# Kernel tuning notes

Measured on AMD Instinct MI355X. Metric: run time of the kernel, lower is better.

Reference implementation:

```python
import jax, jax.numpy as jnp
import numpy as np

D, H, HD, F, A, P, NB, MD = 1024, 16, 64, 2816, 64, 30, 32, 128
B, L = 4, 1024


def _rel_bucket(rel, num_buckets=NB, max_distance=MD):
    # T5 relative position bucket, bidirectional=False (decoder self-attn)
    rel = -jnp.minimum(rel, 0)
    max_exact = num_buckets // 2
    is_small = rel < max_exact
    large = max_exact + (
        jnp.log(jnp.maximum(rel, 1).astype(jnp.float32) / max_exact)
        / np.log(max_distance / max_exact)
        * (num_buckets - max_exact)
    ).astype(jnp.int32)
    large = jnp.minimum(large, num_buckets - 1)
    return jnp.where(is_small, rel, large)


def _rmsnorm(x, scale, eps=1e-6):
    var = jnp.mean(jnp.square(x), axis=-1, keepdims=True)
    return x * jax.lax.rsqrt(var + eps) * scale


def _attn(x, kv, wq, wk, wv, wo, mask, bias, pk, pv):
    # x: [B,Lq,D], kv: [B,Lk,D], prefix pk/pv: [B,P,H,HD]
    hd = wq.shape[-1]
    q = jnp.einsum('bqd,dhe->bqhe', x, wq) * (hd ** -0.5)
    k = jnp.einsum('bkd,dhe->bkhe', kv, wk)
    v = jnp.einsum('bkd,dhe->bkhe', kv, wv)
    k = jnp.concatenate([pk, k], axis=1)  # prefix KV prepended
    v = jnp.concatenate([pv, v], axis=1)
    logits = jnp.einsum('bqhe,bkhe->bhqk', q, k).astype(jnp.float32)
    p = pk.shape[1]
    if bias is not None:
        logits = logits + jnp.pad(bias, ((0, 0), (0, 0), (0, 0), (p, 0)))
    mask = jnp.pad(mask, ((0, 0), (0, 0), (0, 0), (p, 0)), constant_values=True)
    logits = jnp.where(mask, logits, jnp.float32(-1e10))
    w = jax.nn.softmax(logits, axis=-1).astype(x.dtype)
    o = jnp.einsum('bhqk,bkhe->bqhe', w, v)
    return jnp.einsum('bqhe,hed->bqd', o, wo)


def setup_inputs() -> dict:
    key = jax.random.key(0)
    ks = jax.random.split(key, 24)
    s = D ** -0.5
    inp = {
        'inputs': jax.random.normal(ks[0], (B, L, D), jnp.float32),
        'encoded': jax.random.normal(ks[1], (B, L, D), jnp.float32),
        'adapter_wd': jax.random.normal(ks[2], (B, D, A), jnp.float32) * s,
        'adapter_wu': jax.random.normal(ks[3], (B, A, D), jnp.float32) * (A ** -0.5),
        'adapter_bd': jax.random.normal(ks[4], (B, A), jnp.float32) * 0.02,
        'adapter_bu': jax.random.normal(ks[5], (B, D), jnp.float32) * 0.02,
        'prefix_key': jax.random.normal(ks[6], (B, 2, P, H, HD), jnp.float32),
        'prefix_value': jax.random.normal(ks[7], (B, 2, P, H, HD), jnp.float32),
        'ln1': jnp.ones((D,), jnp.float32),
        'ln2': jnp.ones((D,), jnp.float32),
        'ln3': jnp.ones((D,), jnp.float32),
        'sa_wq': jax.random.normal(ks[8], (D, H, HD), jnp.float32) * s,
        'sa_wk': jax.random.normal(ks[9], (D, H, HD), jnp.float32) * s,
        'sa_wv': jax.random.normal(ks[10], (D, H, HD), jnp.float32) * s,
        'sa_wo': jax.random.normal(ks[11], (H, HD, D), jnp.float32) * s,
        'ca_wq': jax.random.normal(ks[12], (D, H, HD), jnp.float32) * s,
        'ca_wk': jax.random.normal(ks[13], (D, H, HD), jnp.float32) * s,
        'ca_wv': jax.random.normal(ks[14], (D, H, HD), jnp.float32) * s,
        'ca_wo': jax.random.normal(ks[15], (H, HD, D), jnp.float32) * s,
        'relpos': jax.random.normal(ks[16], (H, NB), jnp.float32) * 0.1,
        'mlp_wi0': jax.random.normal(ks[17], (D, F), jnp.float32) * s,
        'mlp_wi1': jax.random.normal(ks[18], (D, F), jnp.float32) * s,
        'mlp_wo': jax.random.normal(ks[19], (F, D), jnp.float32) * (F ** -0.5),
        'decoder_mask': jnp.broadcast_to(jnp.tril(jnp.ones((L, L), bool))[None, None], (B, 1, L, L)),
        'encoder_decoder_mask': jnp.ones((B, 1, L, L), bool),
    }
    return inp


def reference(inputs, encoded, adapter_wd, adapter_wu, adapter_bd, adapter_bu,
              prefix_key, prefix_value, ln1, ln2, ln3,
              sa_wq, sa_wk, sa_wv, sa_wo, ca_wq, ca_wk, ca_wv, ca_wo,
              relpos, mlp_wi0, mlp_wi1, mlp_wo,
              decoder_mask, encoder_decoder_mask):
    l = inputs.shape[1]
    pos = jnp.arange(l)
    buckets = _rel_bucket(pos[None, :] - pos[:, None])  # [L,L]
    bias = relpos[:, buckets][None]                      # [1,H,L,L]
    # self-attention with prefix + relative bias
    x = _rmsnorm(inputs, ln1)
    x = _attn(x, x, sa_wq, sa_wk, sa_wv, sa_wo, decoder_mask, bias,
              prefix_key[:, 0], prefix_value[:, 0])
    x = x + inputs
    # cross-attention with prefix
    y = _rmsnorm(x, ln2)
    y = _attn(y, encoded, ca_wq, ca_wk, ca_wv, ca_wo, encoder_decoder_mask, None,
              prefix_key[:, 1], prefix_value[:, 1])
    y = y + x
    # gated-gelu MLP + per-example adapter
    lz = _rmsnorm(y, ln3)
    z = (jax.nn.gelu(lz @ mlp_wi0) * (lz @ mlp_wi1)) @ mlp_wo
    az = jnp.einsum('bld,bda->bla', lz, adapter_wd) + adapter_bd[:, None]
    az = jax.nn.gelu(az)
    az = jnp.einsum('bla,bad->bld', az, adapter_wu) + adapter_bu[:, None]
    z = z + az
    return z + y
```

## Files before the change

### kernel.cpp

```cpp
#include <hip/hip_runtime.h>

typedef unsigned short u16;
typedef __attribute__((ext_vector_type(8))) __bf16 bf16x8;
typedef __attribute__((ext_vector_type(4))) float f32x4;

__device__ __forceinline__ float bf2f(u16 u) {
  union { unsigned int i; float f; } v; v.i = ((unsigned int)u) << 16; return v.f;
}
__device__ __forceinline__ u16 f2bf(float f) {
  unsigned int x = __float_as_uint(f);
  unsigned int r = (x + 0x7fffu + ((x >> 16) & 1u)) >> 16;
  return (u16)r;
}
__device__ __forceinline__ u16 f2bf_fast(float f) {
  return (u16)((__float_as_uint(f) + 0x8000u) >> 16);
}
__device__ __forceinline__ float gelu_f(float x) {
  float u = 0.7978845608028654f * (x + 0.044715f * x * x * x);
  float t = 1.0f - 2.0f / (__expf(2.0f * u) + 1.0f);
  return 0.5f * x * (1.0f + t);
}
__device__ __forceinline__ void gl_lds16(const u16* g, u16* l) {
  __builtin_amdgcn_global_load_lds(
      (const __attribute__((address_space(1))) unsigned int*)g,
// ... 18 lines not shown
  out += (size_t)blockIdx.z * osb;
  int c0 = blockIdx.x * 32, r0 = blockIdx.y * 32;
  int tx = threadIdx.x & 31, ty = threadIdx.x >> 5;
#pragma unroll
  for (int i = 0; i < 4; ++i) {
    int rr = r0 + ty + i * 8;
    if (rr < R && c0 + tx < C) tile[ty + i * 8][tx] = f2bf(in[(size_t)rr * C + c0 + tx]);
  }
  __syncthreads();
#pragma unroll
  for (int i = 0; i < 4; ++i) {
    int cc = c0 + ty + i * 8;
    if (cc < C && r0 + tx < R) out[(size_t)cc * R + r0 + tx] = tile[tx][ty + i * 8];
  }
}

__global__ __launch_bounds__(256) void bias_tab_k(const float* __restrict__ relpos,
                                                  float* __restrict__ tab) {
  int idx = blockIdx.x * 256 + threadIdx.x;
  int h = idx >> 10, d = idx & 1023;
  int bucket;
  if (d < 16) bucket = d;
  else {
    int lb = 16 + (int)(logf((float)d * (1.0f / 16.0f)) * (16.0f / logf(8.0f)));
    bucket = lb < 31 ? lb : 31;
  }
  tab[idx] = relpos[h * 32 + bucket];
}

__global__ __launch_bounds__(256) void prefix_fill_k(
    const float* __restrict__ pK, const float* __restrict__ pV,
    u16* __restrict__ Kd, u16* __restrict__ Vtd, int sSel) {
  int idx = blockIdx.x * 256 + threadIdx.x;
  int e = idx & 63, p = (idx >> 6) & 31, h = (idx >> 11) & 15, b = idx >> 15;
  int key = (p < 30) ? p : (1024 + p);
  float kv = 0.f, vv = 0.f;
  if (p < 30) {
    size_t src = ((((size_t)(b * 2 + sSel)) * 30 + p) * 16 + h) * 64 + e;
    kv = pK[src]; vv = pV[src];
  }
  Kd[(((size_t)(b * 16 + h)) * 1056 + key) * 64 + e] = f2bf(kv);
  Vtd[(((size_t)(b * 16 + h)) * 64 + e) * 1056 + key] = f2bf(vv);
}

__global__ __launch_bounds__(256) void rmsnorm_k(const float* __restrict__ in,
                                                 const float* __restrict__ scale,
                                                 u16* __restrict__ out) {
  const int D = 1024;
  size_t base = (size_t)blockIdx.x * D;
  int t = threadIdx.x;
  float x[4];
#pragma unroll
  for (int i = 0; i < 4; ++i) x[i] = in[base + t + i * 256];
  float s = x[0] * x[0] + x[1] * x[1] + x[2] * x[2] + x[3] * x[3];
#pragma unroll
  for (int off = 1; off < 64; off <<= 1) s += __shfl_xor(s, off, 64);
  __shared__ float ws4[4];
  if ((t & 63) == 0) ws4[t >> 6] = s;
  __syncthreads();
  float tot = ws4[0] + ws4[1] + ws4[2] + ws4[3];
  float r = rsqrtf(tot * (1.0f / D) + 1e-6f);
#pragma unroll
  for (int i = 0; i < 4; ++i) {
    int c = t + i * 256;
    out[base + c] = f2bf(x[i] * r * scale[c]);
  }
}

__global__ __launch_bounds__(256) void gelumul_k(const u16* __restrict__ g2,
                                                 u16* __restrict__ g) {
  int i = blockIdx.x * 256 + threadIdx.x;
  int m = i / 352, f8 = i - m * 352;
  size_t b0 = (size_t)m * 5632 + f8 * 8;
  uint4 h0 = *(const uint4*)(g2 + b0);
  uint4 h1 = *(const uint4*)(g2 + b0 + 2816);
// ... 51 lines not shown
      bf[j] = *(const bf16x8*)&Bs[(wn + j * 16 + fr) * 32 + fq * 8];
#pragma unroll
    for (int i = 0; i < 4; ++i)
#pragma unroll
      for (int j = 0; j < 4; ++j)
        acc[i * 4 + j] = __builtin_amdgcn_mfma_f32_16x16x32_bf16(
            af[i], bf[j], acc[i * 4 + j], 0, 0, 0);
    __syncthreads();
  }

#pragma unroll
  for (int i = 0; i < 4; ++i) {
#pragma unroll
    for (int rr = 0; rr < 4; ++rr) {
      long gm = (long)m0 + wm + i * 16 + fq * 4 + rr;
#pragma unroll
      for (int j = 0; j < 4; ++j) {
        int gn = n0 + wn + j * 16 + fr;
        float v = acc[i * 4 + j][rr];
        size_t oi = (size_t)gm * N + gn;
        if (MODE == 0) ((float*)out)[oi] = v;
        if (MODE == 2) ((u16*)out)[oi] = f2bf(v);
        if (MODE == 3) ((float*)out)[oi] = v + res1[oi];
        if (MODE == 8) {
          int b = (int)(gm >> 10), l = (int)(gm & 1023), h = gn >> 6, e = gn & 63;
          ((u16*)out)[(((size_t)(b * 16 + h)) * 1024 + l) * 64 + e] = f2bf(v * alpha);
        }
        if (MODE == 11) {
          int b = (int)(gm >> 10), l = (int)(gm & 1023);
          int sec = gn >> 10, nn = gn & 1023, h = nn >> 6, e = nn & 63;
          if (sec == 0)
            ((u16*)out)[(((size_t)(b * 16 + h)) * 1024 + l) * 64 + e] = f2bf(v * alpha);
          else if (sec == 1)
            ((u16*)out2)[(((size_t)(b * 16 + h)) * 1056 + 30 + l) * 64 + e] = f2bf(v);
          else
            ((u16*)out3)[(((size_t)(b * 16 + h)) * 64 + e) * 1056 + 30 + l] = f2bf(v);
        }
        if (MODE == 12) {
          int b = (int)(gm >> 10), l = (int)(gm & 1023);
          int sec = gn >> 10, nn = gn & 1023, h = nn >> 6, e = nn & 63;
          if (sec == 0)
            ((u16*)out)[(((size_t)(b * 16 + h)) * 1056 + 30 + l) * 64 + e] = f2bf(v);
          else
            ((u16*)out2)[(((size_t)(b * 16 + h)) * 64 + e) * 1056 + 30 + l] = f2bf(v);
        }
      }
    }
  }
}

template <int MODE>
__global__ __launch_bounds__(256) void gemm_bt(
    const u16* __restrict__ A, const u16* __restrict__ Bt, void* __restrict__ out,
    const float* __restrict__ res1, const float* __restrict__ res2,
    const float* __restrict__ bias, int M, int N, int K,
    long Asb, long Bsb, long bsb, long r1sb, long r2sb, long osb) {
  const int BM = 128, BK = 32, LP = 40;
  __shared__ __align__(16) u16 As[BM * LP];
  __shared__ __align__(16) u16 Bs[BM * LP];

  const int t = threadIdx.x;
  const int m0 = blockIdx.y * BM;
  const int n0 = blockIdx.x * 128;
  const int bz = blockIdx.z;
  A += (size_t)bz * Asb;
  Bt += (size_t)bz * Bsb;

  f32x4 acc[16];
#pragma unroll
  for (int i = 0; i < 16; ++i) acc[i] = (f32x4){0.f, 0.f, 0.f, 0.f};
  const int wave = t >> 6, lane = t & 63;
  const int wm = (wave >> 1) * 64, wn = (wave & 1) * 64;
  const int fr = lane & 15, fq = lane >> 4;

  for (int k0 = 0; k0 < K; k0 += BK) {
#pragma unroll
    for (int i = 0; i < 2; ++i) {
// ... 18 lines not shown
#pragma unroll
      for (int j = 0; j < 4; ++j)
        acc[i * 4 + j] = __builtin_amdgcn_mfma_f32_16x16x32_bf16(
            af[i], bfr[j], acc[i * 4 + j], 0, 0, 0);
    __syncthreads();
  }

#pragma unroll
  for (int i = 0; i < 4; ++i) {
#pragma unroll
    for (int rr = 0; rr < 4; ++rr) {
      long gm = (long)m0 + wm + i * 16 + fq * 4 + rr;
#pragma unroll
      for (int j = 0; j < 4; ++j) {
        int gn = n0 + wn + j * 16 + fr;
        if (gn >= N) continue;
        float v = acc[i * 4 + j][rr];
        size_t oi = (size_t)bz * osb + (size_t)gm * N + gn;
        size_t ri = (size_t)gm * N + gn;
        if (MODE == 6) ((u16*)out)[oi] = f2bf(gelu_f(v + bias[(size_t)bz * bsb + gn]));
        if (MODE == 7)
          ((float*)out)[oi] = v + bias[(size_t)bz * bsb + gn] +
                              res1[(size_t)bz * r1sb + ri] +
                              res2[(size_t)bz * r2sb + ri];
      }
    }
  }
}

template <bool IS_SELF>
__global__ __launch_bounds__(256) void fattn_k(
    const u16* __restrict__ Qg, const u16* __restrict__ Kg,
    const u16* __restrict__ Vtg, const float* __restrict__ bias_tab,
    u16* __restrict__ Out) {
  const int L = 1024, P = 30, KC = 1056;
  const int b = blockIdx.z, h = blockIdx.y, q0b = blockIdx.x * 64;
  const int t = threadIdx.x, wave = t >> 6, lane = t & 63;
  const int fr = lane & 15, fq = lane >> 4;
  const int q0w = q0b + wave * 16;

  __shared__ float bTs[IS_SELF ? 1024 : 4];
  __shared__ __align__(16) u16 Ps[4][16][40];

  if (IS_SELF) {
#pragma unroll
    for (int i = 0; i < 4; ++i) bTs[t + i * 256] = bias_tab[h * 1024 + t + i * 256];
    __syncthreads();
  }

  const u16* qptr = Qg + (((size_t)(b * 16 + h)) * L + q0w + fr) * 64 + fq * 8;
  bf16x8 qa0 = *(const bf16x8*)qptr;
  bf16x8 qa1 = *(const bf16x8*)(qptr + 32);

  f32x4 o[4];
#pragma unroll
  for (int i = 0; i < 4; ++i) o[i] = (f32x4){0.f, 0.f, 0.f, 0.f};
  f32x4 ol = (f32x4){0.f, 0.f, 0.f, 0.f};
  bf16x8 ones;
  {
    u16 one = 0x3F80;
#pragma unroll
    for (int i = 0; i < 8; ++i) ((u16*)&ones)[i] = one;
  }

  const int nk = IS_SELF ? (P + q0b + 64) : (P + L);
  const int nch = (nk + 31) >> 5;
  const u16* kp = Kg + ((size_t)(b * 16 + h)) * KC * 64 + (size_t)fr * 64 + fq * 8;
  const u16* vp = Vtg + ((size_t)(b * 16 + h)) * 64 * KC + (size_t)fr * KC + fq * 8;

  bf16x8 kf0 = *(const bf16x8*)(kp + 0);
  bf16x8 kf1 = *(const bf16x8*)(kp + 32);
  bf16x8 kf2 = *(const bf16x8*)(kp + 16 * 64);
  bf16x8 kf3 = *(const bf16x8*)(kp + 16 * 64 + 32);

  for (int ch = 0; ch < nch; ++ch) {
    const int k0 = ch * 32;
    bf16x8 vf0 = *(const bf16x8*)(vp + 0 * 16 * KC + k0);
    bf16x8 vf1 = *(const bf16x8*)(vp + 1 * 16 * KC + k0);
    bf16x8 vf2 = *(const bf16x8*)(vp + 2 * 16 * KC + k0);
    bf16x8 vf3 = *(const bf16x8*)(vp + 3 * 16 * KC + k0);
    const int k0n = (ch + 1 < nch) ? (k0 + 32) : 0;
    bf16x8 kn0 = *(const bf16x8*)(kp + (size_t)k0n * 64);
    bf16x8 kn1 = *(const bf16x8*)(kp + (size_t)k0n * 64 + 32);
    bf16x8 kn2 = *(const bf16x8*)(kp + (size_t)(k0n + 16) * 64);
    bf16x8 kn3 = *(const bf16x8*)(kp + (size_t)(k0n + 16) * 64 + 32);

    f32x4 s[2];
    s[0] = (f32x4){0.f, 0.f, 0.f, 0.f};
    s[1] = (f32x4){0.f, 0.f, 0.f, 0.f};
    s[0] = __builtin_amdgcn_mfma_f32_16x16x32_bf16(qa0, kf0, s[0], 0, 0, 0);
    s[0] = __builtin_amdgcn_mfma_f32_16x16x32_bf16(qa1, kf1, s[0], 0, 0, 0);
    s[1] = __builtin_amdgcn_mfma_f32_16x16x32_bf16(qa0, kf2, s[1], 0, 0, 0);
    s[1] = __builtin_amdgcn_mfma_f32_16x16x32_bf16(qa1, kf3, s[1], 0, 0, 0);

    const bool full = IS_SELF ? (k0 >= 32 && k0 + 31 - P <= q0w)
                              : (k0 + 31 < P + L);
    if (full) {
      if (IS_SELF) {
#pragma unroll
        for (int reg = 0; reg < 4; ++reg) {
          const int qq = q0w + fq * 4 + reg;
          s[0][reg] += bTs[qq - (k0 + fr - P)];
          s[1][reg] += bTs[qq - (k0 + 16 + fr - P)];
        }
      }
    } else {
#pragma unroll
      for (int reg = 0; reg < 4; ++reg) {
        const int qq = q0w + fq * 4 + reg;
#pragma unroll
        for (int t2 = 0; t2 < 2; ++t2) {
          const int kvi = k0 + t2 * 16 + fr;
          float sv = s[t2][reg];
          if (IS_SELF) {
            const int lk = kvi - P;
            if (lk >= 0) {
              if (lk <= qq) sv += bTs[qq - lk];
              else sv = -3.0e38f;
            }
          } else {
            if (kvi >= P + L) sv = -3.0e38f;
          }
          s[t2][reg] = sv;
        }
      }
    }

#pragma unroll
    for (int reg = 0; reg < 4; ++reg) {
      Ps[wave][fq * 4 + reg][fr] = f2bf_fast(__expf(s[0][reg]));
      Ps[wave][fq * 4 + reg][16 + fr] = f2bf_fast(__expf(s[1][reg]));
    }
    __asm__ volatile("s_waitcnt lgkmcnt(0)" ::: "memory");
    bf16x8 pa = *(const bf16x8*)&Ps[wave][fr][fq * 8];

    o[0] = __builtin_amdgcn_mfma_f32_16x16x32_bf16(pa, vf0, o[0], 0, 0, 0);
    o[1] = __builtin_amdgcn_mfma_f32_16x16x32_bf16(pa, vf1, o[1], 0, 0, 0);
    o[2] = __builtin_amdgcn_mfma_f32_16x16x32_bf16(pa, vf2, o[2], 0, 0, 0);
    o[3] = __builtin_amdgcn_mfma_f32_16x16x32_bf16(pa, vf3, o[3], 0, 0, 0);
    ol   = __builtin_amdgcn_mfma_f32_16x16x32_bf16(pa, ones, ol, 0, 0, 0);

    kf0 = kn0; kf1 = kn1; kf2 = kn2; kf3 = kn3;
  }

  float inv[4];
#pragma unroll
  for (int reg = 0; reg < 4; ++reg) inv[reg] = 1.0f / ol[reg];
#pragma unroll
  for (int dt = 0; dt < 4; ++dt) {
#pragma unroll
    for (int reg = 0; reg < 4; ++reg) {
      size_t oidx =
          (((size_t)(b * L + q0w + fq * 4 + reg)) * 16 + h) * 64 + dt * 16 + fr;
      Out[oidx] = f2bf(o[dt][reg] * inv[reg]);
    }
  }
}

extern "C" void kernel_launch(void* const* d_in, const int* in_sizes, int n_in,
                              void* d_out, int out_size, void* d_ws, size_t ws_size,
                              hipStream_t stream) {
  const int B = 4, L = 1024, D = 1024, H = 16, F = 2816, AD = 64;
  const int M = B * L;
  const int KC = 1056;

  const float* inputs  = (const float*)d_in[0];
  const float* encoded = (const float*)d_in[1];
  const float* a_wd    = (const float*)d_in[2];
  const float* a_wu    = (const float*)d_in[3];
  const float* a_bd    = (const float*)d_in[4];
  const float* a_bu    = (const float*)d_in[5];
  const float* pK      = (const float*)d_in[6];
  const float* pV      = (const float*)d_in[7];
  const float* ln1     = (const float*)d_in[8];
  const float* ln2     = (const float*)d_in[9];
  const float* ln3     = (const float*)d_in[10];
  const float* sa_wq   = (const float*)d_in[11];
  const float* sa_wk   = (const float*)d_in[12];
  const float* sa_wv   = (const float*)d_in[13];
  const float* sa_wo   = (const float*)d_in[14];
  const float* ca_wq   = (const float*)d_in[15];
  const float* ca_wk   = (const float*)d_in[16];
  const float* ca_wv   = (const float*)d_in[17];
  const float* ca_wo   = (const float*)d_in[18];
  const float* relpos  = (const float*)d_in[19];
  const float* wi0     = (const float*)d_in[20];
  const float* wi1     = (const float*)d_in[21];
  const float* wom     = (const float*)d_in[22];

  char* w = (char*)d_ws;
  size_t used = 0;
  auto alloc = [&](size_t bytes) {
    char* p = w + used;
    used += (bytes + 255) & ~(size_t)255;
    return p;
  };
  u16* wqkvT  = (u16*)alloc((size_t)3072 * 1024 * 2);
  u16* woT    = (u16*)alloc((size_t)D * 1024 * 2);
  u16* cqT    = (u16*)alloc((size_t)D * 1024 * 2);
  u16* ckvT   = (u16*)alloc((size_t)2048 * 1024 * 2);
  u16* coT    = (u16*)alloc((size_t)D * 1024 * 2);
  u16* wi01T  = (u16*)alloc((size_t)5632 * 1024 * 2);
  u16* womT   = (u16*)alloc((size_t)D * F * 2);
  u16* wdT    = (u16*)alloc((size_t)B * AD * D * 2);
  u16* wuT    = (u16*)alloc((size_t)B * D * AD * 2);
  float* bT   = (float*)alloc((size_t)H * 1024 * 4);
  u16* enc16  = (u16*)alloc((size_t)M * D * 2);
  u16* xn     = (u16*)alloc((size_t)M * D * 2);
  u16* lz     = (u16*)alloc((size_t)M * D * 2);
  u16* Kc     = (u16*)alloc((size_t)B * H * KC * 64 * 2);
  u16* Vtc    = (u16*)alloc((size_t)B * H * 64 * KC * 2);
  u16* qh     = (u16*)alloc((size_t)B * H * L * 64 * 2);
  u16* ao     = (u16*)alloc((size_t)M * D * 2);
  float* xf   = (float*)alloc((size_t)M * D * 4);
  float* yf   = (float*)alloc((size_t)M * D * 4);
  u16* az1    = (u16*)alloc((size_t)B * 1024 * AD * 2);
  u16* g2     = Kc;
  u16* g      = enc16;
  float* zf   = (float*)Kc;
  if (used > ws_size) return;

  dim3 tb(256);
  auto T = [&](const float* src, u16* dst, int R, int C, int nb, long sb) {
    transpose_k<<<dim3((C + 31) / 32, (R + 31) / 32, nb), tb, 0, stream>>>(
        src, dst, R, C, sb, sb);
  };
  T(sa_wq, wqkvT, D, 1024, 1, 0);
  T(sa_wk, wqkvT + (size_t)1024 * 1024, D, 1024, 1, 0);
  T(sa_wv, wqkvT + (size_t)2048 * 1024, D, 1024, 1, 0);
  T(sa_wo, woT, 1024, D, 1, 0);
  T(ca_wq, cqT, D, 1024, 1, 0);
  T(ca_wk, ckvT, D, 1024, 1, 0);
  T(ca_wv, ckvT + (size_t)1024 * 1024, D, 1024, 1, 0);
  T(ca_wo, coT, 1024, D, 1, 0);
  T(wi0, wi01T, D, F, 1, 0);
  T(wi1, wi01T + (size_t)2816 * 1024, D, F, 1, 0);
  T(wom, womT, F, D, 1, 0);
  T(a_wd, wdT, D, AD, B, (long)D * AD);
  T(a_wu, wuT, AD, D, B, (long)AD * D);
  bias_tab_k<<<dim3(64), tb, 0, stream>>>(relpos, bT);
  cast_bf16_k<<<dim3(M * D / 4 / 256), tb, 0, stream>>>(encoded, enc16, M * D / 4);

#define G97(MODE, Ap, Btp, Op, O2, O3, R1, Nn, Kk, al)                         \
  gemm97<MODE><<<dim3((Nn) / 128, M / 128), tb, 0, stream>>>(                  \
      (const u16*)(Ap), (const u16*)(Btp), (void*)(Op), (void*)(O2),           \
      (void*)(O3), (const float*)(R1), M, Nn, Kk, al)

  rmsnorm_k<<<dim3(M), tb, 0, stream>>>(inputs, ln1, xn);
  G97(11, xn, wqkvT, qh, Kc, Vtc, nullptr, 3072, D, 0.125f);
  prefix_fill_k<<<dim3(512), tb, 0, stream>>>(pK, pV, Kc, Vtc, 0);
  fattn_k<true><<<dim3(L / 64, H, B), tb, 0, stream>>>(qh, Kc, Vtc, bT, ao);
  G97(3, ao, woT, xf, nullptr, nullptr, inputs, 1024, D, 1.f);
  rmsnorm_k<<<dim3(M), tb, 0, stream>>>(xf, ln2, xn);
  G97(8, xn, cqT, qh, nullptr, nullptr, nullptr, 1024, D, 0.125f);
  G97(12, enc16, ckvT, Kc, Vtc, nullptr, nullptr, 2048, D, 1.f);
  prefix_fill_k<<<dim3(512), tb, 0, stream>>>(pK, pV, Kc, Vtc, 1);
  fattn_k<false><<<dim3(L / 64, H, B), tb, 0, stream>>>(qh, Kc, Vtc, nullptr, ao);
  G97(3, ao, coT, yf, nullptr, nullptr, xf, 1024, D, 1.f);
  rmsnorm_k<<<dim3(M), tb, 0, stream>>>(yf, ln3, lz);
  gemm_bt<6><<<dim3(1, 8, B), tb, 0, stream>>>(
      lz, wdT, az1, nullptr, nullptr, a_bd, 1024, AD, D,
      (long)1024 * D, (long)AD * D, (long)AD, 0, 0, (long)1024 * AD);
  G97(2, lz, wi01T, g2, nullptr, nullptr, nullptr, 5632, D, 1.f);
  gelumul_k<<<dim3(5632), tb, 0, stream>>>(g2, g);
  G97(0, g, womT, zf, nullptr, nullptr, nullptr, 1024, F, 1.f);
  gemm_bt<7><<<dim3(8, 8, B), tb, 0, stream>>>(
      az1, wuT, d_out, zf, yf, a_bu, 1024, 1024, AD,
      (long)1024 * AD, (long)D * AD, (long)1024, (long)1024 * 1024,
      (long)1024 * 1024, (long)1024 * 1024);
#undef G97
  (void)in_sizes; (void)n_in; (void)out_size;
}
```

Measured before the change: 828.1 us.

## Process 64-key chunks in flash attention with MFMA priority and XCD-aware block swizzle

The attention kernel now handles two 32-key sub-chunks per iteration. That doubles the in-flight K/V register loads and MFMA work per loop trip, and the P staging buffer is double-buffered in LDS. K/V padding grows from 1056 to 1088 keys so the 64-wide chunks stay in bounds, and the prefix fill and GEMM epilogues change to match. It also adds s_setprio around the MFMA groups and remaps a flat 1D grid so that blocks of the same batch/head land on the same XCD for L2 reuse. The costs are higher register pressure and extra padded work on the last chunk.

Result: slower. 873.8 us (+5.5%).

```diff
diff --git a/kernel.cpp b/kernel.cpp
--- a/kernel.cpp
+++ b/kernel.cpp
@@ -74,15 +74,15 @@
     const float* __restrict__ pK, const float* __restrict__ pV,
     u16* __restrict__ Kd, u16* __restrict__ Vtd, int sSel) {
   int idx = blockIdx.x * 256 + threadIdx.x;
-  int e = idx & 63, p = (idx >> 6) & 31, h = (idx >> 11) & 15, b = idx >> 15;
+  int e = idx & 63, p = (idx >> 6) & 63, h = (idx >> 12) & 15, b = idx >> 16;
   int key = (p < 30) ? p : (1024 + p);
   float kv = 0.f, vv = 0.f;
   if (p < 30) {
     size_t src = ((((size_t)(b * 2 + sSel)) * 30 + p) * 16 + h) * 64 + e;
     kv = pK[src]; vv = pV[src];
   }
-  Kd[(((size_t)(b * 16 + h)) * 1056 + key) * 64 + e] = f2bf(kv);
-  Vtd[(((size_t)(b * 16 + h)) * 64 + e) * 1056 + key] = f2bf(vv);
+  Kd[(((size_t)(b * 16 + h)) * 1088 + key) * 64 + e] = f2bf(kv);
+  Vtd[(((size_t)(b * 16 + h)) * 64 + e) * 1088 + key] = f2bf(vv);
 }
 
 __global__ __launch_bounds__(256) void rmsnorm_k(const float* __restrict__ in,
@@ -200,17 +200,17 @@
           if (sec == 0)
             ((u16*)out)[(((size_t)(b * 16 + h)) * 1024 + l) * 64 + e] = f2bf(v * alpha);
           else if (sec == 1)
-            ((u16*)out2)[(((size_t)(b * 16 + h)) * 1056 + 30 + l) * 64 + e] = f2bf(v);
+            ((u16*)out2)[(((size_t)(b * 16 + h)) * 1088 + 30 + l) * 64 + e] = f2bf(v);
           else
-            ((u16*)out3)[(((size_t)(b * 16 + h)) * 64 + e) * 1056 + 30 + l] = f2bf(v);
+            ((u16*)out3)[(((size_t)(b * 16 + h)) * 64 + e) * 1088 + 30 + l] = f2bf(v);
         }
         if (MODE == 12) {
           int b = (int)(gm >> 10), l = (int)(gm & 1023);
           int sec = gn >> 10, nn = gn & 1023, h = nn >> 6, e = nn & 63;
           if (sec == 0)
-            ((u16*)out)[(((size_t)(b * 16 + h)) * 1056 + 30 + l) * 64 + e] = f2bf(v);
+            ((u16*)out)[(((size_t)(b * 16 + h)) * 1088 + 30 + l) * 64 + e] = f2bf(v);
           else
-            ((u16*)out2)[(((size_t)(b * 16 + h)) * 64 + e) * 1056 + 30 + l] = f2bf(v);
+            ((u16*)out2)[(((size_t)(b * 16 + h)) * 64 + e) * 1088 + 30 + l] = f2bf(v);
         }
       }
     }
@@ -296,14 +296,17 @@
     const u16* __restrict__ Qg, const u16* __restrict__ Kg,
     const u16* __restrict__ Vtg, const float* __restrict__ bias_tab,
     u16* __restrict__ Out) {
-  const int L = 1024, P = 30, KC = 1056;
-  const int b = blockIdx.z, h = blockIdx.y, q0b = blockIdx.x * 64;
+  const int L = 1024, P = 30, KC = 1088;
+  const int flat = blockIdx.x;
+  const int wg = (flat & 7) * 128 + (flat >> 3);
+  const int q0b = (wg & 15) * 64;
+  const int h = (wg >> 4) & 15, b = wg >> 8;
   const int t = threadIdx.x, wave = t >> 6, lane = t & 63;
   const int fr = lane & 15, fq = lane >> 4;
   const int q0w = q0b + wave * 16;
 
   __shared__ float bTs[IS_SELF ? 1024 : 4];
-  __shared__ __align__(16) u16 Ps[4][16][40];
+  __shared__ __align__(16) u16 Ps[4][2][16][40];
 
   if (IS_SELF) {
 #pragma unroll
@@ -327,44 +330,29 @@
   }
 
   const int nk = IS_SELF ? (P + q0b + 64) : (P + L);
-  const int nch = (nk + 31) >> 5;
+  const int nit = (nk + 63) >> 6;
   const u16* kp = Kg + ((size_t)(b * 16 + h)) * KC * 64 + (size_t)fr * 64 + fq * 8;
   const u16* vp = Vtg + ((size_t)(b * 16 + h)) * 64 * KC + (size_t)fr * KC + fq * 8;
 
-  bf16x8 kf0 = *(const bf16x8*)(kp + 0);
-  bf16x8 kf1 = *(const bf16x8*)(kp + 32);
-  bf16x8 kf2 = *(const bf16x8*)(kp + 16 * 64);
-  bf16x8 kf3 = *(const bf16x8*)(kp + 16 * 64 + 32);
-
-  for (int ch = 0; ch < nch; ++ch) {
-    const int k0 = ch * 32;
-    bf16x8 vf0 = *(const bf16x8*)(vp + 0 * 16 * KC + k0);
-    bf16x8 vf1 = *(const bf16x8*)(vp + 1 * 16 * KC + k0);
-    bf16x8 vf2 = *(const bf16x8*)(vp + 2 * 16 * KC + k0);
-    bf16x8 vf3 = *(const bf16x8*)(vp + 3 * 16 * KC + k0);
-    const int k0n = (ch + 1 < nch) ? (k0 + 32) : 0;
-    bf16x8 kn0 = *(const bf16x8*)(kp + (size_t)k0n * 64);
-    bf16x8 kn1 = *(const bf16x8*)(kp + (size_t)k0n * 64 + 32);
-    bf16x8 kn2 = *(const bf16x8*)(kp + (size_t)(k0n + 16) * 64);
-    bf16x8 kn3 = *(const bf16x8*)(kp + (size_t)(k0n + 16) * 64 + 32);
-
-    f32x4 s[2];
-    s[0] = (f32x4){0.f, 0.f, 0.f, 0.f};
-    s[1] = (f32x4){0.f, 0.f, 0.f, 0.f};
-    s[0] = __builtin_amdgcn_mfma_f32_16x16x32_bf16(qa0, kf0, s[0], 0, 0, 0);
-    s[0] = __builtin_amdgcn_mfma_f32_16x16x32_bf16(qa1, kf1, s[0], 0, 0, 0);
-    s[1] = __builtin_amdgcn_mfma_f32_16x16x32_bf16(qa0, kf2, s[1], 0, 0, 0);
-    s[1] = __builtin_amdgcn_mfma_f32_16x16x32_bf16(qa1, kf3, s[1], 0, 0, 0);
-
-    const bool full = IS_SELF ? (k0 >= 32 && k0 + 31 - P <= q0w)
-                              : (k0 + 31 < P + L);
+  bf16x8 ka0 = *(const bf16x8*)(kp + 0);
+  bf16x8 ka1 = *(const bf16x8*)(kp + 32);
+  bf16x8 ka2 = *(const bf16x8*)(kp + 16 * 64);
+  bf16x8 ka3 = *(const bf16x8*)(kp + 16 * 64 + 32);
+  bf16x8 kb0 = *(const bf16x8*)(kp + 32 * 64);
+  bf16x8 kb1 = *(const bf16x8*)(kp + 32 * 64 + 32);
+  bf16x8 kb2 = *(const bf16x8*)(kp + 48 * 64);
+  bf16x8 kb3 = *(const bf16x8*)(kp + 48 * 64 + 32);
+
+  auto smax = [&](f32x4* s, int kk0, int cidx) {
+    const bool full = IS_SELF ? (kk0 >= 32 && kk0 + 31 - P <= q0w)
+                              : (kk0 + 31 < P + L);
     if (full) {
       if (IS_SELF) {
 #pragma unroll
         for (int reg = 0; reg < 4; ++reg) {
           const int qq = q0w + fq * 4 + reg;
-          s[0][reg] += bTs[qq - (k0 + fr - P)];
-          s[1][reg] += bTs[qq - (k0 + 16 + fr - P)];
+          s[0][reg] += bTs[qq - (kk0 + fr - P)];
+          s[1][reg] += bTs[qq - (kk0 + 16 + fr - P)];
         }
       }
     } else {
@@ -373,7 +361,7 @@
         const int qq = q0w + fq * 4 + reg;
 #pragma unroll
         for (int t2 = 0; t2 < 2; ++t2) {
-          const int kvi = k0 + t2 * 16 + fr;
+          const int kvi = kk0 + t2 * 16 + fr;
           float sv = s[t2][reg];
           if (IS_SELF) {
             const int lk = kvi - P;
@@ -388,22 +376,68 @@
         }
       }
     }
-
 #pragma unroll
     for (int reg = 0; reg < 4; ++reg) {
-      Ps[wave][fq * 4 + reg][fr] = f2bf_fast(__expf(s[0][reg]));
-      Ps[wave][fq * 4 + reg][16 + fr] = f2bf_fast(__expf(s[1][reg]));
+      Ps[wave][cidx][fq * 4 + reg][fr] = f2bf_fast(__expf(s[0][reg]));
+      Ps[wave][cidx][fq * 4 + reg][16 + fr] = f2bf_fast(__expf(s[1][reg]));
     }
+  };
+
+  for (int it = 0; it < nit; ++it) {
+    const int k0 = it * 64;
+    bf16x8 va0 = *(const bf16x8*)(vp + 0 * 16 * KC + k0);
+    bf16x8 va1 = *(const bf16x8*)(vp + 1 * 16 * KC + k0);
+    bf16x8 va2 = *(const bf16x8*)(vp + 2 * 16 * KC + k0);
+    bf16x8 va3 = *(const bf16x8*)(vp + 3 * 16 * KC + k0);
+    bf16x8 vb0 = *(const bf16x8*)(vp + 0 * 16 * KC + k0 + 32);
+    bf16x8 vb1 = *(const bf16x8*)(vp + 1 * 16 * KC + k0 + 32);
+    bf16x8 vb2 = *(const bf16x8*)(vp + 2 * 16 * KC + k0 + 32);
+    bf16x8 vb3 = *(const bf16x8*)(vp + 3 * 16 * KC + k0 + 32);
+
+    f32x4 sA[2], sB[2];
+    sA[0] = (f32x4){0.f, 0.f, 0.f, 0.f};
+    sA[1] = (f32x4){0.f, 0.f, 0.f, 0.f};
+    sB[0] = (f32x4){0.f, 0.f, 0.f, 0.f};
+    sB[1] = (f32x4){0.f, 0.f, 0.f, 0.f};
+    __builtin_amdgcn_s_setprio(1);
+    sA[0] = __builtin_amdgcn_mfma_f32_16x16x32_bf16(qa0, ka0, sA[0], 0, 0, 0);
+    sA[0] = __builtin_amdgcn_mfma_f32_16x16x32_bf16(qa1, ka1, sA[0], 0, 0, 0);
+    sA[1] = __builtin_amdgcn_mfma_f32_16x16x32_bf16(qa0, ka2, sA[1], 0, 0, 0);
+    sA[1] = __builtin_amdgcn_mfma_f32_16x16x32_bf16(qa1, ka3, sA[1], 0, 0, 0);
+    sB[0] = __builtin_amdgcn_mfma_f32_16x16x32_bf16(qa0, kb0, sB[0], 0, 0, 0);
+    sB[0] = __builtin_amdgcn_mfma_f32_16x16x32_bf16(qa1, kb1, sB[0], 0, 0, 0);
+    sB[1] = __builtin_amdgcn_mfma_f32_16x16x32_bf16(qa0, kb2, sB[1], 0, 0, 0);
+    sB[1] = __builtin_amdgcn_mfma_f32_16x16x32_bf16(qa1, kb3, sB[1], 0, 0, 0);
+    __builtin_amdgcn_s_setprio(0);
+
+    const int k0n = (it + 1 < nit) ? (k0 + 64) : 0;
+    ka0 = *(const bf16x8*)(kp + (size_t)k0n * 64);
+    ka1 = *(const bf16x8*)(kp + (size_t)k0n * 64 + 32);
+    ka2 = *(const bf16x8*)(kp + (size_t)(k0n + 16) * 64);
+    ka3 = *(const bf16x8*)(kp + (size_t)(k0n + 16) * 64 + 32);
+    kb0 = *(const bf16x8*)(kp + (size_t)(k0n + 32) * 64);
+    kb1 = *(const bf16x8*)(kp + (size_t)(k0n + 32) * 64 + 32);
+    kb2 = *(const bf16x8*)(kp + (size_t)(k0n + 48) * 64);
+    kb3 = *(const bf16x8*)(kp + (size_t)(k0n + 48) * 64 + 32);
+
+    smax(sA, k0, 0);
+    smax(sB, k0 + 32, 1);
     __asm__ volatile("s_waitcnt lgkmcnt(0)" ::: "memory");
-    bf16x8 pa = *(const bf16x8*)&Ps[wave][fr][fq * 8];
-
-    o[0] = __builtin_amdgcn_mfma_f32_16x16x32_bf16(pa, vf0, o[0], 0, 0, 0);
-    o[1] = __builtin_amdgcn_mfma_f32_16x16x32_bf16(pa, vf1, o[1], 0, 0, 0);
-    o[2] = __builtin_amdgcn_mfma_f32_16x16x32_bf16(pa, vf2, o[2], 0, 0, 0);
-    o[3] = __builtin_amdgcn_mfma_f32_16x16x32_bf16(pa, vf3, o[3], 0, 0, 0);
-    ol   = __builtin_amdgcn_mfma_f32_16x16x32_bf16(pa, ones, ol, 0, 0, 0);
-
-    kf0 = kn0; kf1 = kn1; kf2 = kn2; kf3 = kn3;
+    bf16x8 paA = *(const bf16x8*)&Ps[wave][0][fr][fq * 8];
+    bf16x8 paB = *(const bf16x8*)&Ps[wave][1][fr][fq * 8];
+
+    __builtin_amdgcn_s_setprio(1);
+    o[0] = __builtin_amdgcn_mfma_f32_16x16x32_bf16(paA, va0, o[0], 0, 0, 0);
+    o[1] = __builtin_amdgcn_mfma_f32_16x16x32_bf16(paA, va1, o[1], 0, 0, 0);
+    o[2] = __builtin_amdgcn_mfma_f32_16x16x32_bf16(paA, va2, o[2], 0, 0, 0);
+    o[3] = __builtin_amdgcn_mfma_f32_16x16x32_bf16(paA, va3, o[3], 0, 0, 0);
+    ol   = __builtin_amdgcn_mfma_f32_16x16x32_bf16(paA, ones, ol, 0, 0, 0);
+    o[0] = __builtin_amdgcn_mfma_f32_16x16x32_bf16(paB, vb0, o[0], 0, 0, 0);
+    o[1] = __builtin_amdgcn_mfma_f32_16x16x32_bf16(paB, vb1, o[1], 0, 0, 0);
+    o[2] = __builtin_amdgcn_mfma_f32_16x16x32_bf16(paB, vb2, o[2], 0, 0, 0);
+    o[3] = __builtin_amdgcn_mfma_f32_16x16x32_bf16(paB, vb3, o[3], 0, 0, 0);
+    ol   = __builtin_amdgcn_mfma_f32_16x16x32_bf16(paB, ones, ol, 0, 0, 0);
+    __builtin_amdgcn_s_setprio(0);
   }
 
   float inv[4];
@@ -425,7 +459,7 @@
                               hipStream_t stream) {
   const int B = 4, L = 1024, D = 1024, H = 16, F = 2816, AD = 64;
   const int M = B * L;
-  const int KC = 1056;
+  const int KC = 1088;
 
   const float* inputs  = (const float*)d_in[0];
   const float* encoded = (const float*)d_in[1];
@@ -511,14 +545,14 @@
 
   rmsnorm_k<<<dim3(M), tb, 0, stream>>>(inputs, ln1, xn);
   G97(11, xn, wqkvT, qh, Kc, Vtc, nullptr, 3072, D, 0.125f);
-  prefix_fill_k<<<dim3(512), tb, 0, stream>>>(pK, pV, Kc, Vtc, 0);
-  fattn_k<true><<<dim3(L / 64, H, B), tb, 0, stream>>>(qh, Kc, Vtc, bT, ao);
+  prefix_fill_k<<<dim3(1024), tb, 0, stream>>>(pK, pV, Kc, Vtc, 0);
+  fattn_k<true><<<dim3(1024), tb, 0, stream>>>(qh, Kc, Vtc, bT, ao);
   G97(3, ao, woT, xf, nullptr, nullptr, inputs, 1024, D, 1.f);
   rmsnorm_k<<<dim3(M), tb, 0, stream>>>(xf, ln2, xn);
   G97(8, xn, cqT, qh, nullptr, nullptr, nullptr, 1024, D, 0.125f);
   G97(12, enc16, ckvT, Kc, Vtc, nullptr, nullptr, 2048, D, 1.f);
-  prefix_fill_k<<<dim3(512), tb, 0, stream>>>(pK, pV, Kc, Vtc, 1);
-  fattn_k<false><<<dim3(L / 64, H, B), tb, 0, stream>>>(qh, Kc, Vtc, nullptr, ao);
+  prefix_fill_k<<<dim3(1024), tb, 0, stream>>>(pK, pV, Kc, Vtc, 1);
+  fattn_k<false><<<dim3(1024), tb, 0, stream>>>(qh, Kc, Vtc, nullptr, ao);
   G97(3, ao, coT, yf, nullptr, nullptr, xf, 1024, D, 1.f);
   rmsnorm_k<<<dim3(M), tb, 0, stream>>>(yf, ln3, lz);
   gemm_bt<6><<<dim3(1, 8, B), tb, 0, stream>>>(
```

## Split attention key range across two workgroups and merge partials in a combine kernel

Applied to the files above, without the earlier changes.

Each attention workgroup now covers only half of the key chunks for its query tile. It writes unnormalized fp32 partial outputs and row sums to scratch, and a new combine kernel adds the two halves, normalizes, and stores bf16. This doubles the grid and evens out the causal work imbalance in self-attention. Block indices are also remapped (an XCD-style swizzle) so neighbouring tiles share caches. The cost is extra fp32 traffic and one more launch per attention. Partial buffers reuse other workspace regions, and the xn buffer is smaller than the partial output it now holds, so that buffer spills into the adjacent allocation.

After: 831.6 us. Within noise of the previous version (+0.4%).

```diff
diff --git a/kernel.cpp b/kernel.cpp
--- a/kernel.cpp
+++ b/kernel.cpp
@@ -295,12 +295,19 @@
 __global__ __launch_bounds__(256) void fattn_k(
     const u16* __restrict__ Qg, const u16* __restrict__ Kg,
     const u16* __restrict__ Vtg, const float* __restrict__ bias_tab,
-    u16* __restrict__ Out) {
+    float* __restrict__ o0P, float* __restrict__ o1P,
+    float* __restrict__ l0P, float* __restrict__ l1P) {
   const int L = 1024, P = 30, KC = 1056;
-  const int b = blockIdx.z, h = blockIdx.y, q0b = blockIdx.x * 64;
+  const int flat = blockIdx.x;
+  const int wg = (flat & 7) * 256 + (flat >> 3);
+  const int half = wg & 1;
+  const int q0b = ((wg >> 1) & 15) * 64;
+  const int h = (wg >> 5) & 15, b = wg >> 9;
   const int t = threadIdx.x, wave = t >> 6, lane = t & 63;
   const int fr = lane & 15, fq = lane >> 4;
   const int q0w = q0b + wave * 16;
+  float* __restrict__ oP = half ? o1P : o0P;
+  float* __restrict__ lP = half ? l1P : l0P;
 
   __shared__ float bTs[IS_SELF ? 1024 : 4];
   __shared__ __align__(16) u16 Ps[4][16][40];
@@ -327,22 +334,25 @@
   }
 
   const int nk = IS_SELF ? (P + q0b + 64) : (P + L);
-  const int nch = (nk + 31) >> 5;
+  const int ncht = (nk + 31) >> 5;
+  const int c0 = half ? (ncht >> 1) : 0;
+  const int c1 = half ? ncht : (ncht >> 1);
   const u16* kp = Kg + ((size_t)(b * 16 + h)) * KC * 64 + (size_t)fr * 64 + fq * 8;
   const u16* vp = Vtg + ((size_t)(b * 16 + h)) * 64 * KC + (size_t)fr * KC + fq * 8;
 
-  bf16x8 kf0 = *(const bf16x8*)(kp + 0);
-  bf16x8 kf1 = *(const bf16x8*)(kp + 32);
-  bf16x8 kf2 = *(const bf16x8*)(kp + 16 * 64);
-  bf16x8 kf3 = *(const bf16x8*)(kp + 16 * 64 + 32);
-
-  for (int ch = 0; ch < nch; ++ch) {
+  const int kb = c0 * 32;
+  bf16x8 kf0 = *(const bf16x8*)(kp + (size_t)kb * 64);
+  bf16x8 kf1 = *(const bf16x8*)(kp + (size_t)kb * 64 + 32);
+  bf16x8 kf2 = *(const bf16x8*)(kp + (size_t)(kb + 16) * 64);
+  bf16x8 kf3 = *(const bf16x8*)(kp + (size_t)(kb + 16) * 64 + 32);
+
+  for (int ch = c0; ch < c1; ++ch) {
     const int k0 = ch * 32;
     bf16x8 vf0 = *(const bf16x8*)(vp + 0 * 16 * KC + k0);
     bf16x8 vf1 = *(const bf16x8*)(vp + 1 * 16 * KC + k0);
     bf16x8 vf2 = *(const bf16x8*)(vp + 2 * 16 * KC + k0);
     bf16x8 vf3 = *(const bf16x8*)(vp + 3 * 16 * KC + k0);
-    const int k0n = (ch + 1 < nch) ? (k0 + 32) : 0;
+    const int k0n = (ch + 1 < c1) ? (k0 + 32) : 0;
     bf16x8 kn0 = *(const bf16x8*)(kp + (size_t)k0n * 64);
     bf16x8 kn1 = *(const bf16x8*)(kp + (size_t)k0n * 64 + 32);
     bf16x8 kn2 = *(const bf16x8*)(kp + (size_t)(k0n + 16) * 64);
@@ -406,18 +416,42 @@
     kf0 = kn0; kf1 = kn1; kf2 = kn2; kf3 = kn3;
   }
 
-  float inv[4];
-#pragma unroll
-  for (int reg = 0; reg < 4; ++reg) inv[reg] = 1.0f / ol[reg];
 #pragma unroll
   for (int dt = 0; dt < 4; ++dt) {
 #pragma unroll
     for (int reg = 0; reg < 4; ++reg) {
       size_t oidx =
-          (((size_t)(b * L + q0w + fq * 4 + reg)) * 16 + h) * 64 + dt * 16 + fr;
-      Out[oidx] = f2bf(o[dt][reg] * inv[reg]);
+          (((size_t)(b * 16 + h)) * 1024 + q0w + fq * 4 + reg) * 64 + dt * 16 + fr;
+      oP[oidx] = o[dt][reg];
     }
   }
+  if (fr == 0) {
+#pragma unroll
+    for (int reg = 0; reg < 4; ++reg)
+      lP[((size_t)(b * 16 + h)) * 1024 + q0w + fq * 4 + reg] = ol[reg];
+  }
+}
+
+__global__ __launch_bounds__(256) void attn_comb_k(
+    const float* __restrict__ o0, const float* __restrict__ o1,
+    const float* __restrict__ l0, const float* __restrict__ l1,
+    u16* __restrict__ Out) {
+  const int bh = blockIdx.x >> 6;
+  const int q0 = (blockIdx.x & 63) * 16;
+  const int t = threadIdx.x;
+  const int qi = q0 + (t >> 4), dq = (t & 15) * 4;
+  const size_t row = (size_t)bh * 1024 + qi;
+  const size_t src = row * 64 + dq;
+  float4 a = *(const float4*)(o0 + src);
+  float4 c = *(const float4*)(o1 + src);
+  float inv = 1.0f / (l0[row] + l1[row]);
+  ushort4 ov;
+  ov.x = f2bf((a.x + c.x) * inv);
+  ov.y = f2bf((a.y + c.y) * inv);
+  ov.z = f2bf((a.z + c.z) * inv);
+  ov.w = f2bf((a.w + c.w) * inv);
+  const int bb = bh >> 4, hh = bh & 15;
+  *(ushort4*)(Out + ((((size_t)bb * 1024 + qi) * 16 + hh) * 64 + dq)) = ov;
 }
 
 extern "C" void kernel_launch(void* const* d_in, const int* in_sizes, int n_in,
@@ -481,6 +515,10 @@
   u16* g2     = Kc;
   u16* g      = enc16;
   float* zf   = (float*)Kc;
+  float* oh0  = yf;
+  float* oh1  = (float*)xn;
+  float* lh0  = (float*)az1;
+  float* lh1  = lh0 + 65536;
   if (used > ws_size) return;
 
   dim3 tb(256);
@@ -512,13 +550,15 @@
   rmsnorm_k<<<dim3(M), tb, 0, stream>>>(inputs, ln1, xn);
   G97(11, xn, wqkvT, qh, Kc, Vtc, nullptr, 3072, D, 0.125f);
   prefix_fill_k<<<dim3(512), tb, 0, stream>>>(pK, pV, Kc, Vtc, 0);
-  fattn_k<true><<<dim3(L / 64, H, B), tb, 0, stream>>>(qh, Kc, Vtc, bT, ao);
+  fattn_k<true><<<dim3(2048), tb, 0, stream>>>(qh, Kc, Vtc, bT, oh0, oh1, lh0, lh1);
+  attn_comb_k<<<dim3(4096), tb, 0, stream>>>(oh0, oh1, lh0, lh1, ao);
   G97(3, ao, woT, xf, nullptr, nullptr, inputs, 1024, D, 1.f);
   rmsnorm_k<<<dim3(M), tb, 0, stream>>>(xf, ln2, xn);
   G97(8, xn, cqT, qh, nullptr, nullptr, nullptr, 1024, D, 0.125f);
   G97(12, enc16, ckvT, Kc, Vtc, nullptr, nullptr, 2048, D, 1.f);
   prefix_fill_k<<<dim3(512), tb, 0, stream>>>(pK, pV, Kc, Vtc, 1);
-  fattn_k<false><<<dim3(L / 64, H, B), tb, 0, stream>>>(qh, Kc, Vtc, nullptr, ao);
+  fattn_k<false><<<dim3(2048), tb, 0, stream>>>(qh, Kc, Vtc, nullptr, oh0, oh1, lh0, lh1);
+  attn_comb_k<<<dim3(4096), tb, 0, stream>>>(oh0, oh1, lh0, lh1, ao);
   G97(3, ao, coT, yf, nullptr, nullptr, xf, 1024, D, 1.f);
   rmsnorm_k<<<dim3(M), tb, 0, stream>>>(yf, ln3, lz);
   gemm_bt<6><<<dim3(1, 8, B), tb, 0, stream>>>(
```

## Process 32 query rows per wave in flash attention and remap block order

Applied to the files above, without the earlier changes.

Each wave now handles two 16-row query tiles that share every K and V fragment load, so K/V global traffic per query is halved. A block covers 128 queries instead of 64, and the grid is flattened to 512 blocks with an XCD-aware swizzle so neighbouring blocks go to the same chiplet. The cost is more accumulator registers and half as many blocks. Causal blocks also get coarser, so more fully masked chunks are computed and workload imbalance grows.

Measured after the change: 754.2 us. -8.9%, faster.

```diff
diff --git a/kernel.cpp b/kernel.cpp
--- a/kernel.cpp
+++ b/kernel.cpp
@@ -297,13 +297,16 @@
     const u16* __restrict__ Vtg, const float* __restrict__ bias_tab,
     u16* __restrict__ Out) {
   const int L = 1024, P = 30, KC = 1056;
-  const int b = blockIdx.z, h = blockIdx.y, q0b = blockIdx.x * 64;
+  const int flat = blockIdx.x;
+  const int wg = (flat & 7) * 64 + (flat >> 3);
+  const int q0b = (wg & 7) * 128;
+  const int h = (wg >> 3) & 15, b = wg >> 7;
   const int t = threadIdx.x, wave = t >> 6, lane = t & 63;
   const int fr = lane & 15, fq = lane >> 4;
-  const int q0w = q0b + wave * 16;
+  const int q0w = q0b + wave * 32;
 
   __shared__ float bTs[IS_SELF ? 1024 : 4];
-  __shared__ __align__(16) u16 Ps[4][16][40];
+  __shared__ __align__(16) u16 Ps[4][32][40];
 
   if (IS_SELF) {
 #pragma unroll
@@ -314,11 +317,17 @@
   const u16* qptr = Qg + (((size_t)(b * 16 + h)) * L + q0w + fr) * 64 + fq * 8;
   bf16x8 qa0 = *(const bf16x8*)qptr;
   bf16x8 qa1 = *(const bf16x8*)(qptr + 32);
-
-  f32x4 o[4];
-#pragma unroll
-  for (int i = 0; i < 4; ++i) o[i] = (f32x4){0.f, 0.f, 0.f, 0.f};
-  f32x4 ol = (f32x4){0.f, 0.f, 0.f, 0.f};
+  bf16x8 qb0 = *(const bf16x8*)(qptr + 16 * 64);
+  bf16x8 qb1 = *(const bf16x8*)(qptr + 16 * 64 + 32);
+
+  f32x4 oA[4], oB[4];
+#pragma unroll
+  for (int i = 0; i < 4; ++i) {
+    oA[i] = (f32x4){0.f, 0.f, 0.f, 0.f};
+    oB[i] = (f32x4){0.f, 0.f, 0.f, 0.f};
+  }
+  f32x4 olA = (f32x4){0.f, 0.f, 0.f, 0.f};
+  f32x4 olB = (f32x4){0.f, 0.f, 0.f, 0.f};
   bf16x8 ones;
   {
     u16 one = 0x3F80;
@@ -326,7 +335,7 @@
     for (int i = 0; i < 8; ++i) ((u16*)&ones)[i] = one;
   }
 
-  const int nk = IS_SELF ? (P + q0b + 64) : (P + L);
+  const int nk = IS_SELF ? (P + q0b + 128) : (P + L);
   const int nch = (nk + 31) >> 5;
   const u16* kp = Kg + ((size_t)(b * 16 + h)) * KC * 64 + (size_t)fr * 64 + fq * 8;
   const u16* vp = Vtg + ((size_t)(b * 16 + h)) * 64 * KC + (size_t)fr * KC + fq * 8;
@@ -336,33 +345,14 @@
   bf16x8 kf2 = *(const bf16x8*)(kp + 16 * 64);
   bf16x8 kf3 = *(const bf16x8*)(kp + 16 * 64 + 32);
 
-  for (int ch = 0; ch < nch; ++ch) {
-    const int k0 = ch * 32;
-    bf16x8 vf0 = *(const bf16x8*)(vp + 0 * 16 * KC + k0);
-    bf16x8 vf1 = *(const bf16x8*)(vp + 1 * 16 * KC + k0);
-    bf16x8 vf2 = *(const bf16x8*)(vp + 2 * 16 * KC + k0);
-    bf16x8 vf3 = *(const bf16x8*)(vp + 3 * 16 * KC + k0);
-    const int k0n = (ch + 1 < nch) ? (k0 + 32) : 0;
-    bf16x8 kn0 = *(const bf16x8*)(kp + (size_t)k0n * 64);
-    bf16x8 kn1 = *(const bf16x8*)(kp + (size_t)k0n * 64 + 32);
-    bf16x8 kn2 = *(const bf16x8*)(kp + (size_t)(k0n + 16) * 64);
-    bf16x8 kn3 = *(const bf16x8*)(kp + (size_t)(k0n + 16) * 64 + 32);
-
-    f32x4 s[2];
-    s[0] = (f32x4){0.f, 0.f, 0.f, 0.f};
-    s[1] = (f32x4){0.f, 0.f, 0.f, 0.f};
-    s[0] = __builtin_amdgcn_mfma_f32_16x16x32_bf16(qa0, kf0, s[0], 0, 0, 0);
-    s[0] = __builtin_amdgcn_mfma_f32_16x16x32_bf16(qa1, kf1, s[0], 0, 0, 0);
-    s[1] = __builtin_amdgcn_mfma_f32_16x16x32_bf16(qa0, kf2, s[1], 0, 0, 0);
-    s[1] = __builtin_amdgcn_mfma_f32_16x16x32_bf16(qa1, kf3, s[1], 0, 0, 0);
-
-    const bool full = IS_SELF ? (k0 >= 32 && k0 + 31 - P <= q0w)
+  auto smax = [&](f32x4* s, int k0, int qoff, int rb) {
+    const bool full = IS_SELF ? (k0 >= 32 && k0 + 31 - P <= qoff)
                               : (k0 + 31 < P + L);
     if (full) {
       if (IS_SELF) {
 #pragma unroll
         for (int reg = 0; reg < 4; ++reg) {
-          const int qq = q0w + fq * 4 + reg;
+          const int qq = qoff + fq * 4 + reg;
           s[0][reg] += bTs[qq - (k0 + fr - P)];
           s[1][reg] += bTs[qq - (k0 + 16 + fr - P)];
         }
@@ -370,7 +360,7 @@
     } else {
 #pragma unroll
       for (int reg = 0; reg < 4; ++reg) {
-        const int qq = q0w + fq * 4 + reg;
+        const int qq = qoff + fq * 4 + reg;
 #pragma unroll
         for (int t2 = 0; t2 < 2; ++t2) {
           const int kvi = k0 + t2 * 16 + fr;
@@ -388,34 +378,73 @@
         }
       }
     }
-
 #pragma unroll
     for (int reg = 0; reg < 4; ++reg) {
-      Ps[wave][fq * 4 + reg][fr] = f2bf_fast(__expf(s[0][reg]));
-      Ps[wave][fq * 4 + reg][16 + fr] = f2bf_fast(__expf(s[1][reg]));
+      Ps[wave][rb + fq * 4 + reg][fr] = f2bf_fast(__expf(s[0][reg]));
+      Ps[wave][rb + fq * 4 + reg][16 + fr] = f2bf_fast(__expf(s[1][reg]));
     }
+  };
+
+  for (int ch = 0; ch < nch; ++ch) {
+    const int k0 = ch * 32;
+    bf16x8 vf0 = *(const bf16x8*)(vp + 0 * 16 * KC + k0);
+    bf16x8 vf1 = *(const bf16x8*)(vp + 1 * 16 * KC + k0);
+    bf16x8 vf2 = *(const bf16x8*)(vp + 2 * 16 * KC + k0);
+    bf16x8 vf3 = *(const bf16x8*)(vp + 3 * 16 * KC + k0);
+    const int k0n = (ch + 1 < nch) ? (k0 + 32) : 0;
+    bf16x8 kn0 = *(const bf16x8*)(kp + (size_t)k0n * 64);
+    bf16x8 kn1 = *(const bf16x8*)(kp + (size_t)k0n * 64 + 32);
+    bf16x8 kn2 = *(const bf16x8*)(kp + (size_t)(k0n + 16) * 64);
+    bf16x8 kn3 = *(const bf16x8*)(kp + (size_t)(k0n + 16) * 64 + 32);
+
+    f32x4 sA[2], sB[2];
+    sA[0] = (f32x4){0.f, 0.f, 0.f, 0.f};
+    sA[1] = (f32x4){0.f, 0.f, 0.f, 0.f};
+    sB[0] = (f32x4){0.f, 0.f, 0.f, 0.f};
+    sB[1] = (f32x4){0.f, 0.f, 0.f, 0.f};
+    sA[0] = __builtin_amdgcn_mfma_f32_16x16x32_bf16(qa0, kf0, sA[0], 0, 0, 0);
+    sA[0] = __builtin_amdgcn_mfma_f32_16x16x32_bf16(qa1, kf1, sA[0], 0, 0, 0);
+    sA[1] = __builtin_amdgcn_mfma_f32_16x16x32_bf16(qa0, kf2, sA[1], 0, 0, 0);
+    sA[1] = __builtin_amdgcn_mfma_f32_16x16x32_bf16(qa1, kf3, sA[1], 0, 0, 0);
+    sB[0] = __builtin_amdgcn_mfma_f32_16x16x32_bf16(qb0, kf0, sB[0], 0, 0, 0);
+    sB[0] = __builtin_amdgcn_mfma_f32_16x16x32_bf16(qb1, kf1, sB[0], 0, 0, 0);
+    sB[1] = __builtin_amdgcn_mfma_f32_16x16x32_bf16(qb0, kf2, sB[1], 0, 0, 0);
+    sB[1] = __builtin_amdgcn_mfma_f32_16x16x32_bf16(qb1, kf3, sB[1], 0, 0, 0);
+
+    smax(sA, k0, q0w, 0);
+    smax(sB, k0, q0w + 16, 16);
     __asm__ volatile("s_waitcnt lgkmcnt(0)" ::: "memory");
-    bf16x8 pa = *(const bf16x8*)&Ps[wave][fr][fq * 8];
-
-    o[0] = __builtin_amdgcn_mfma_f32_16x16x32_bf16(pa, vf0, o[0], 0, 0, 0);
-    o[1] = __builtin_amdgcn_mfma_f32_16x16x32_bf16(pa, vf1, o[1], 0, 0, 0);
-    o[2] = __builtin_amdgcn_mfma_f32_16x16x32_bf16(pa, vf2, o[2], 0, 0, 0);
-    o[3] = __builtin_amdgcn_mfma_f32_16x16x32_bf16(pa, vf3, o[3], 0, 0, 0);
-    ol   = __builtin_amdgcn_mfma_f32_16x16x32_bf16(pa, ones, ol, 0, 0, 0);
+    bf16x8 paA = *(const bf16x8*)&Ps[wave][fr][fq * 8];
+    bf16x8 paB = *(const bf16x8*)&Ps[wave][16 + fr][fq * 8];
+
+    oA[0] = __builtin_amdgcn_mfma_f32_16x16x32_bf16(paA, vf0, oA[0], 0, 0, 0);
+    oA[1] = __builtin_amdgcn_mfma_f32_16x16x32_bf16(paA, vf1, oA[1], 0, 0, 0);
+    oA[2] = __builtin_amdgcn_mfma_f32_16x16x32_bf16(paA, vf2, oA[2], 0, 0, 0);
+    oA[3] = __builtin_amdgcn_mfma_f32_16x16x32_bf16(paA, vf3, oA[3], 0, 0, 0);
+    olA   = __builtin_amdgcn_mfma_f32_16x16x32_bf16(paA, ones, olA, 0, 0, 0);
+    oB[0] = __builtin_amdgcn_mfma_f32_16x16x32_bf16(paB, vf0, oB[0], 0, 0, 0);
+    oB[1] = __builtin_amdgcn_mfma_f32_16x16x32_bf16(paB, vf1, oB[1], 0, 0, 0);
+    oB[2] = __builtin_amdgcn_mfma_f32_16x16x32_bf16(paB, vf2, oB[2], 0, 0, 0);
+    oB[3] = __builtin_amdgcn_mfma_f32_16x16x32_bf16(paB, vf3, oB[3], 0, 0, 0);
+    olB   = __builtin_amdgcn_mfma_f32_16x16x32_bf16(paB, ones, olB, 0, 0, 0);
 
     kf0 = kn0; kf1 = kn1; kf2 = kn2; kf3 = kn3;
   }
 
-  float inv[4];
-#pragma unroll
-  for (int reg = 0; reg < 4; ++reg) inv[reg] = 1.0f / ol[reg];
+  float invA[4], invB[4];
+#pragma unroll
+  for (int reg = 0; reg < 4; ++reg) {
+    invA[reg] = 1.0f / olA[reg];
+    invB[reg] = 1.0f / olB[reg];
+  }
 #pragma unroll
   for (int dt = 0; dt < 4; ++dt) {
 #pragma unroll
     for (int reg = 0; reg < 4; ++reg) {
-      size_t oidx =
-          (((size_t)(b * L + q0w + fq * 4 + reg)) * 16 + h) * 64 + dt * 16 + fr;
-      Out[oidx] = f2bf(o[dt][reg] * inv[reg]);
+      size_t rowA = (size_t)(b * L + q0w + fq * 4 + reg);
+      Out[(rowA * 16 + h) * 64 + dt * 16 + fr] = f2bf(oA[dt][reg] * invA[reg]);
+      size_t rowB = rowA + 16;
+      Out[(rowB * 16 + h) * 64 + dt * 16 + fr] = f2bf(oB[dt][reg] * invB[reg]);
     }
   }
 }
@@ -512,13 +541,13 @@
   rmsnorm_k<<<dim3(M), tb, 0, stream>>>(inputs, ln1, xn);
   G97(11, xn, wqkvT, qh, Kc, Vtc, nullptr, 3072, D, 0.125f);
   prefix_fill_k<<<dim3(512), tb, 0, stream>>>(pK, pV, Kc, Vtc, 0);
-  fattn_k<true><<<dim3(L / 64, H, B), tb, 0, stream>>>(qh, Kc, Vtc, bT, ao);
+  fattn_k<true><<<dim3(512), tb, 0, stream>>>(qh, Kc, Vtc, bT, ao);
   G97(3, ao, woT, xf, nullptr, nullptr, inputs, 1024, D, 1.f);
   rmsnorm_k<<<dim3(M), tb, 0, stream>>>(xf, ln2, xn);
   G97(8, xn, cqT, qh, nullptr, nullptr, nullptr, 1024, D, 0.125f);
   G97(12, enc16, ckvT, Kc, Vtc, nullptr, nullptr, 2048, D, 1.f);
   prefix_fill_k<<<dim3(512), tb, 0, stream>>>(pK, pV, Kc, Vtc, 1);
-  fattn_k<false><<<dim3(L / 64, H, B), tb, 0, stream>>>(qh, Kc, Vtc, nullptr, ao);
+  fattn_k<false><<<dim3(512), tb, 0, stream>>>(qh, Kc, Vtc, nullptr, ao);
   G97(3, ao, coT, yf, nullptr, nullptr, xf, 1024, D, 1.f);
   rmsnorm_k<<<dim3(M), tb, 0, stream>>>(yf, ln3, lz);
   gemm_bt<6><<<dim3(1, 8, B), tb, 0, stream>>>(
```
